# Kernel tuning notes

Measured on AMD Instinct MI355X. Metric: run time of the kernel, lower is better.

Reference implementation:

```python
import jax, jax.numpy as jnp
import numpy as np

N_NODES = 100000
N_EDGES = 800000


def gcn_conv(x, W, b, src, dst, ew, n):
    # PyG GCNConv with edge weights and self-loops already included in (src, dst, ew):
    # deg[i] = sum of incoming edge weights at i; norm_e = d^-1/2[src] * w_e * d^-1/2[dst]
    h = x @ W                                                  # [N, F_out]
    deg = jax.ops.segment_sum(ew, dst, num_segments=n)         # [N]
    dinv = jnp.where(deg > 0, jax.lax.rsqrt(deg), 0.0)
    norm = dinv[src] * ew * dinv[dst]                          # [E]
    out = jax.ops.segment_sum(h[src] * norm[:, None], dst, num_segments=n)
    return out + b


def add_self_loops(edge_index, edge_weight, n):
    loop = jnp.arange(n, dtype=edge_index.dtype)
    src = jnp.concatenate([edge_index[0], loop])
    dst = jnp.concatenate([edge_index[1], loop])
    ew = jnp.concatenate([edge_weight, jnp.ones((n,), edge_weight.dtype)])
    return src, dst, ew


def setup_inputs() -> dict:
    key = jax.random.key(0)
    ks = jax.random.split(key, 10)
    x = jax.random.normal(ks[0], (N_NODES, 5), jnp.float32)
    edge_index = jax.random.randint(ks[1], (2, N_EDGES), 0, N_NODES, dtype=jnp.int64)
    edge_weight = jax.random.uniform(ks[2], (N_EDGES,), jnp.float32)
    def glorot(k, fan_in, fan_out):
        s = float(np.sqrt(6.0 / (fan_in + fan_out)))
        return jax.random.uniform(k, (fan_in, fan_out), jnp.float32, -s, s)
    return {
        "x": x,
        "edge_index": edge_index,
        "edge_weight": edge_weight,
        "W1": glorot(ks[3], 5, 320),
        "b1": jnp.zeros((320,), jnp.float32),
        "W2": glorot(ks[4], 320, 160),
        "b2": jnp.zeros((160,), jnp.float32),
        "We": glorot(ks[5], 160, 80),
        "be": jnp.zeros((80,), jnp.float32),
    }


def reference(x, edge_index, edge_weight, W1, b1, W2, b2, We, be):
    n = x.shape[0]
    src, dst, ew = add_self_loops(edge_index, edge_weight, n)
    h = gcn_conv(x, W1, b1, src, dst, ew, n)        # conv1
    h = jax.nn.relu(h)
    h = gcn_conv(h, W2, b2, src, dst, ew, n)        # conv2
    return h @ We + be                              # embed linear
```

## Files before the change

### kernel.cpp

```cpp
#include <hip/hip_runtime.h>

#define NF0 5
#define F1 320
#define F2 160
#define F3 80
#define NSUB 8
#define SUBCAP 512

typedef float f32x4 __attribute__((ext_vector_type(4)));
typedef _Float16 f16x8 __attribute__((ext_vector_type(8)));


__global__ void k_init(int* __restrict__ zreg, int zwords,
                       const unsigned int* __restrict__ ei32, int E, int* __restrict__ flag) {
    for (int t = blockIdx.x * 256 + threadIdx.x; t < zwords; t += gridDim.x * 256)
        zreg[t] = 0;
    if (blockIdx.x == 0) {
        __shared__ int ok;
        if (threadIdx.x == 0) ok = 1;
        __syncthreads();
        int np = E < 2048 ? E : 2048;
        for (int i = threadIdx.x; i < np; i += 256)
            if (ei32[2 * i + 1] != 0u) ok = 0;
        __syncthreads();
        if (threadIdx.x == 0) *flag = ok;
    }
}


__global__ void k_binA(const void* ei, const float* __restrict__ ew, const int* __restrict__ flag,
                       int* __restrict__ bin_cnt , int2* __restrict__ bins,
                       int n_bins, int* __restrict__ ovf_n, int* __restrict__ ovf,
                       int ovf_cap, int E) {
    int e = blockIdx.x * blockDim.x + threadIdx.x;
    if (e >= E) return;
    int sub = blockIdx.x & (NSUB - 1);
    int s, d;
    if (*flag) {
        const long long* p = (const long long*)ei;
        s = (int)p[e]; d = (int)p[E + e];
    } else {
        const int* p = (const int*)ei;
        s = p[e]; d = p[E + e];
    }
    float w = ew[e];
    int b = d >> 8;
    int pos = atomicAdd(&bin_cnt[(sub * n_bins + b) * 4], 1);
    if (pos < SUBCAP) {
        int2 pk;
        pk.x = s | ((d & 255) << 24);
        pk.y = __float_as_int(w);
        bins[(size_t)b * (NSUB * SUBCAP) + sub * SUBCAP + pos] = pk;
    } else {
        int o = atomicAdd(ovf_n, 1);
        if (o < ovf_cap) {
            ovf[3 * o] = s; ovf[3 * o + 1] = d; ovf[3 * o + 2] = __float_as_int(w);
        }
    }
}


__global__ __launch_bounds__(512) void k_binB1x(const int2* __restrict__ bins,
                                                const int* __restrict__ bin_cnt, int n_bins,
                                                float* __restrict__ dinv,
                                                const int* __restrict__ ovf_n,
                                                const int* __restrict__ ovf, int ovf_cap, int N,
                                                const float* __restrict__ W2,
                                                const float* __restrict__ We,
                                                _Float16* __restrict__ Bh,
                                                const float* __restrict__ b2,
                                                const float* __restrict__ be,
                                                float* __restrict__ bc) {
    __shared__ float deg_l[256];
    int b = blockIdx.x, t = threadIdx.x;
    if (b >= n_bins) {
        int xb = b - n_bins;
        if (xb < 50) {
            int idx = xb * 512 + t;
            int fid = idx >> 9;
            int rem = idx & 511;
            int lane = rem >> 3, i = rem & 7;
            int kk = fid / 5, ct = fid - kk * 5;
            int col = ct * 16 + (lane & 15);
            int row = kk * 32 + (lane >> 4) * 8 + i;
            const float* wr = W2 + (size_t)row * F2;
            float acc = 0.f;
            #pragma unroll 4
            for (int m = 0; m < F2; m += 4) {
                float4 w4 = *(const float4*)(wr + m);
                acc += w4.x * We[m * F3 + col] + w4.y * We[(m + 1) * F3 + col]
                     + w4.z * We[(m + 2) * F3 + col] + w4.w * We[(m + 3) * F3 + col];
            }
            Bh[((size_t)fid * 64 + lane) * 8 + i] = (_Float16)acc;
        } else {
            if (t < F3) {
                float s = be[t];
                for (int k = 0; k < F2; ++k) s += b2[k] * We[k * F3 + t];
                bc[t] = s;
            }
        }
        return;
    }
    if (t < 256) deg_l[t] = 0.f;
    __syncthreads();
    int th = t >> 8;
    int tt = t & 255;
    for (int sp = 0; sp < NSUB; sp += 2) {
        int sub = sp + th;
        int ne = bin_cnt[(sub * n_bins + b) * 4]; if (ne > SUBCAP) ne = SUBCAP;
        const int2* bp = bins + (size_t)b * (NSUB * SUBCAP) + sub * SUBCAP;
        for (int j = tt; j < ne; j += 256) {
            int2 pk = bp[j];
            atomicAdd(&deg_l[((unsigned int)pk.x) >> 24], __int_as_float(pk.y));
        }
    }
    int n = *ovf_n; if (n > ovf_cap) n = ovf_cap;
    int lo = b * 256;
    for (int j = t; j < n; j += 512) {
        int d = ovf[3 * j + 1];
        if (d >= lo && d < lo + 256)
            atomicAdd(&deg_l[d - lo], __int_as_float(ovf[3 * j + 2]));
    }
    __syncthreads();
    int node = lo + t;
    if (t < 256 && node < N) dinv[node] = rsqrtf(1.0f + deg_l[t]);
}


__global__ __launch_bounds__(512) void k_binB2(const int2* __restrict__ bins,
                                               const int* __restrict__ bin_cnt, int n_bins,
                                               const float* __restrict__ dinv,
                                               const float* __restrict__ x,
                                               int* __restrict__ cnt, int2* __restrict__ bucket,
                                               int cap, float* __restrict__ agg1,
                                               int* __restrict__ ovf_n, int* __restrict__ ovf,
                                               int ovf_cap, int N) {
    __shared__ int cnt_l[256];
    __shared__ float acc_l[256 * NF0];
    int b = blockIdx.x, t = threadIdx.x;
    if (t < 256) cnt_l[t] = 0;
    for (int q = t; q < 256 * NF0; q += 512) acc_l[q] = 0.f;
    int nsnap = *ovf_n; if (nsnap > ovf_cap) nsnap = ovf_cap;
    __syncthreads();
    int lo = b * 256;

    for (int j = t; j < nsnap; j += 512) {
        int d = ovf[3 * j + 1];
        if (d >= lo && d < lo + 256) {
            int s = ovf[3 * j];
            float w = __int_as_float(ovf[3 * j + 2]) * dinv[s];
            const float* xs = x + (size_t)s * NF0;
            int dl = d - lo;
            #pragma unroll
            for (int f = 0; f < NF0; ++f)
                atomicAdd(&acc_l[dl * NF0 + f], xs[f] * w);
        }
    }

    int th = t >> 8;
    int tt = t & 255;
    for (int sp = 0; sp < NSUB; sp += 2) {
        int sub = sp + th;
        int ne = bin_cnt[(sub * n_bins + b) * 4]; if (ne > SUBCAP) ne = SUBCAP;
        const int2* bp = bins + (size_t)b * (NSUB * SUBCAP) + sub * SUBCAP;
        for (int j = tt; j < ne; j += 256) {
            int2 pk = bp[j];
            int s = pk.x & 0xFFFFFF;
            int dl = ((unsigned int)pk.x) >> 24;
            int node = lo + dl;
            int pos = atomicAdd(&cnt_l[dl], 1);
            if (pos < cap) {
                int2 out_pk; out_pk.x = s; out_pk.y = pk.y;
                bucket[(size_t)node * cap + pos] = out_pk;
            } else {
                int o = atomicAdd(ovf_n, 1);
                if (o < ovf_cap) { ovf[3 * o] = s; ovf[3 * o + 1] = node; ovf[3 * o + 2] = pk.y; }
            }
            float w = __int_as_float(pk.y) * dinv[s];
            const float* xs = x + (size_t)s * NF0;
            float4 sv = *(const float4*)xs;
            float s4 = xs[4];
            atomicAdd(&acc_l[dl * NF0 + 0], sv.x * w);
            atomicAdd(&acc_l[dl * NF0 + 1], sv.y * w);
            atomicAdd(&acc_l[dl * NF0 + 2], sv.z * w);
            atomicAdd(&acc_l[dl * NF0 + 3], sv.w * w);
            atomicAdd(&acc_l[dl * NF0 + 4], s4 * w);
        }
    }
    __syncthreads();

    int node = lo + t;
    if (t < 256 && node < N) {
        float di = dinv[node];
        float sc = di * di;
        const float* xn = x + (size_t)node * NF0;
        float* op = agg1 + (size_t)node * NF0;
        #pragma unroll
        for (int f = 0; f < NF0; ++f)
            op[f] = di * acc_l[t * NF0 + f] + sc * xn[f];
        int c = cnt_l[t]; if (c > cap) c = cap;
        cnt[node] = c;
    }
}


__global__ __launch_bounds__(512) void k_node(const float* __restrict__ agg1,
                                              const float* __restrict__ W1,
                                              const float* __restrict__ b1,
                                              const _Float16* __restrict__ Bh,
                                              const float* __restrict__ dinv,
                                              _Float16* __restrict__ g, int N) {
    __shared__ float W_l[6 * F1];
    __shared__ _Float16 B_l[50 * 64 * 8];
    int tid = threadIdx.x;
    if (tid < 480) {
        float4 v = (tid < 400) ? ((const float4*)W1)[tid] : ((const float4*)b1)[tid - 400];
        ((float4*)W_l)[tid] = v;
    }
    {
        const float4* src = (const float4*)Bh;
        float4* dst = (float4*)B_l;
        for (int i = tid; i < 3200; i += 512) dst[i] = src[i];
    }
    __syncthreads();

    int w = tid >> 6, l = tid & 63;
    int nl = l & 15, kg = l >> 4;
    int base = blockIdx.x * 128 + w * 16;
    int n0 = base + nl;

    float a0v[5] = {0.f, 0.f, 0.f, 0.f, 0.f};
    if (n0 < N) {
        const float* ap = agg1 + (size_t)n0 * NF0;
        #pragma unroll
        for (int j = 0; j < 5; ++j) a0v[j] = ap[j];
    }

    f32x4 zero = {0.f, 0.f, 0.f, 0.f};
    f32x4 acc[5] = {zero, zero, zero, zero, zero};
    const f16x8* blp = (const f16x8*)B_l;

    #pragma unroll
    for (int kk = 0; kk < 10; ++kk) {
        int k0 = kk * 32 + kg * 8;
        float v0[8];
        const float* bb = W_l + 5 * F1 + k0;
        #pragma unroll
        for (int i = 0; i < 8; ++i) v0[i] = bb[i];
        #pragma unroll
        for (int j = 0; j < 5; ++j) {
            const float* wp = W_l + j * F1 + k0;
            float aj0 = a0v[j];
            #pragma unroll
            for (int i = 0; i < 8; ++i) v0[i] += aj0 * wp[i];
        }
        f16x8 ah0;
        #pragma unroll
        for (int i = 0; i < 8; ++i)
            ah0[i] = (_Float16)fmaxf(v0[i], 0.f);
        #pragma unroll
        for (int ct = 0; ct < 5; ++ct) {
            f16x8 bf = blp[(kk * 5 + ct) * 64 + l];
            acc[ct] = __builtin_amdgcn_mfma_f32_16x16x32_f16(ah0, bf, acc[ct], 0, 0, 0);
        }
    }

    #pragma unroll
    for (int r = 0; r < 4; ++r) {
        int r0 = base + kg * 4 + r;
        if (r0 < N) {
            float dv = dinv[r0];
            #pragma unroll
            for (int ct = 0; ct < 5; ++ct)
                g[(size_t)r0 * F3 + ct * 16 + nl] = (_Float16)(acc[ct][r] * dv);
        }
    }
}


__global__ __launch_bounds__(256) void k_aggB(const _Float16* __restrict__ g,
                                              const float* __restrict__ dinv,
                                              const float* __restrict__ bc,
                                              const int* __restrict__ cnt,
                                              const int2* __restrict__ bucket, int cap,
                                              const int* __restrict__ ovf_n,
                                              const int* __restrict__ ovf, int ovf_cap,
                                              float* __restrict__ out, int N) {
    int t = blockIdx.x * blockDim.x + threadIdx.x;
    if (t >= 10 * N) return;
    int i = t / 10;
    int c = (t - i * 10) << 3;
    float acc[8];
    #pragma unroll
    for (int e = 0; e < 8; ++e) acc[e] = 0.f;
    int cn = cnt[i];
    const int4* row4 = (const int4*)(bucket + (size_t)i * cap);
    int j = 0;
    for (; j + 2 <= cn; j += 2) {
        int4 q = row4[j >> 1];
        float w0 = __int_as_float(q.y);
        float w1 = __int_as_float(q.w);
        f16x8 a0 = *(const f16x8*)(g + (size_t)q.x * F3 + c);
        f16x8 a1 = *(const f16x8*)(g + (size_t)q.z * F3 + c);
        #pragma unroll
        for (int e = 0; e < 8; ++e)
            acc[e] += (float)a0[e] * w0 + (float)a1[e] * w1;
    }
    if (j < cn) {
        int2 p0 = ((const int2*)row4)[j];
        float w0 = __int_as_float(p0.y);
        f16x8 a0 = *(const f16x8*)(g + (size_t)p0.x * F3 + c);
        #pragma unroll
        for (int e = 0; e < 8; ++e)
            acc[e] += (float)a0[e] * w0;
    }
    {
        int n = *ovf_n; if (n > ovf_cap) n = ovf_cap;
        for (int o = 0; o < n; ++o) {
            if (ovf[3 * o + 1] == i) {
                int s = ovf[3 * o];
                float w0 = __int_as_float(ovf[3 * o + 2]);
                f16x8 a0 = *(const f16x8*)(g + (size_t)s * F3 + c);
                #pragma unroll
                for (int e = 0; e < 8; ++e)
                    acc[e] += (float)a0[e] * w0;
            }
        }
    }
    float di = dinv[i];
    f16x8 u0 = *(const f16x8*)(g + (size_t)i * F3 + c);
    const f32x4* bp = (const f32x4*)(bc + c);
    f32x4 q0 = bp[0], q1 = bp[1];
    f32x4 o0, o1;
    o0.x = di * (acc[0] + (float)u0[0]) + q0.x;
    o0.y = di * (acc[1] + (float)u0[1]) + q0.y;
    o0.z = di * (acc[2] + (float)u0[2]) + q0.z;
    o0.w = di * (acc[3] + (float)u0[3]) + q0.w;
    o1.x = di * (acc[4] + (float)u0[4]) + q1.x;
    o1.y = di * (acc[5] + (float)u0[5]) + q1.y;
    o1.z = di * (acc[6] + (float)u0[6]) + q1.z;
    o1.w = di * (acc[7] + (float)u0[7]) + q1.w;
    f32x4* op = (f32x4*)(out + (size_t)i * F3 + c);
    __builtin_nontemporal_store(o0, op);
    __builtin_nontemporal_store(o1, op + 1);
}


static inline size_t align256(size_t x) { return (x + 255) & ~(size_t)255; }

extern "C" void kernel_launch(void* const* d_in, const int* in_sizes, int n_in,
                              void* d_out, int out_size, void* d_ws, size_t ws_size,
                              hipStream_t stream) {
    const float* x  = (const float*)d_in[0];
    const void*  ei = d_in[1];
    const float* ew = (const float*)d_in[2];
    const float* W1 = (const float*)d_in[3];
    const float* b1 = (const float*)d_in[4];
    const float* W2 = (const float*)d_in[5];
    const float* b2 = (const float*)d_in[6];
    const float* We = (const float*)d_in[7];
    const float* be = (const float*)d_in[8];
    float* out = (float*)d_out;

    int N = in_sizes[0] / NF0;
    int E = in_sizes[2];

    const int OVF_CAP = 131072;
    int n_bins = (N + 255) >> 8;

    char* p = (char*)d_ws;
    auto alloc = [&](size_t bytes) { char* r = p; p += align256(bytes); return r; };
    int*   flag  = (int*)alloc(4);
    int zwords = 16 + NSUB * n_bins * 4;
    int*   zreg  = (int*)alloc((size_t)zwords * 4);
    int*   ovf_n = zreg;
    int*   bin_cnt = zreg + 16;
    float* dinv  = (float*)alloc((size_t)N * 4);
    int*   cnt   = (int*)  alloc((size_t)N * 4);
    int*   ovf   = (int*)  alloc((size_t)OVF_CAP * 12);
    int2*  bins  = (int2*) alloc((size_t)n_bins * NSUB * SUBCAP * 8);
    float* agg1  = (float*)alloc((size_t)N * NF0 * 4);
    float* bc    = (float*)alloc((size_t)F3 * 4);
    _Float16* Bh = (_Float16*)alloc((size_t)50 * 64 * 8 * 2);
    _Float16* g  = (_Float16*)alloc((size_t)N * F3 * 2);

    size_t used = (size_t)(p - (char*)d_ws);
    int cap = 24;
    if (ws_size > used) {
        size_t avail = (ws_size - used) / ((size_t)N * 8);
        if (avail < (size_t)cap) cap = (int)avail;
    } else cap = 4;
    cap &= ~1;
    if (cap < 4) cap = 4;
    int2* bucket = (int2*)alloc((size_t)N * cap * 8);

    int eb   = (E + 255) / 256;
    int zb   = (zwords + 255) / 256;

    k_init<<<zb, 256, 0, stream>>>(zreg, zwords, (const unsigned int*)ei, E, flag);
    k_binA<<<eb, 256, 0, stream>>>(ei, ew, flag, bin_cnt, bins, n_bins, ovf_n, ovf, OVF_CAP, E);
    k_binB1x<<<n_bins + 51, 512, 0, stream>>>(bins, bin_cnt, n_bins, dinv, ovf_n, ovf, OVF_CAP, N,
                                              W2, We, Bh, b2, be, bc);
    k_binB2<<<n_bins, 512, 0, stream>>>(bins, bin_cnt, n_bins, dinv, x, cnt, bucket, cap,
                                        agg1, ovf_n, ovf, OVF_CAP, N);
    k_node<<<(N + 127) / 128, 512, 0, stream>>>(agg1, W1, b1, Bh, dinv, g, N);
    k_aggB<<<(10 * N + 255) / 256, 256, 0, stream>>>(g, dinv, bc, cnt, bucket, cap,
                                                     ovf_n, ovf, OVF_CAP, out, N);
}
```

Measured before the change: 155.2 us.

## Prescale node features by dinv into padded buffer; read W1 directly in k_node

k_binB1x now writes a per-node copy of x pre-multiplied by dinv, padded to 8 floats, so k_binB2's edge loop no longer gathers dinv[s] and reads aligned 32-byte rows. The self-loop term becomes di*(acc + xp). Separately, k_node drops its W1/b1 shared-memory staging, reads those weights through vector global loads (cache-resident), and adds an occupancy hint of 6. The cost is an extra 3.2MB buffer write and more global load traffic in k_node.

After: 171.3 us. +10.4%, slower.

```diff
diff --git a/kernel.cpp b/kernel.cpp
--- a/kernel.cpp
+++ b/kernel.cpp
@@ -63,6 +63,8 @@
 __global__ __launch_bounds__(512) void k_binB1x(const int2* __restrict__ bins,
                                                 const int* __restrict__ bin_cnt, int n_bins,
                                                 float* __restrict__ dinv,
+                                                const float* __restrict__ x,
+                                                float* __restrict__ xp,
                                                 const int* __restrict__ ovf_n,
                                                 const int* __restrict__ ovf, int ovf_cap, int N,
                                                 const float* __restrict__ W2,
@@ -123,14 +125,23 @@
     }
     __syncthreads();
     int node = lo + t;
-    if (t < 256 && node < N) dinv[node] = rsqrtf(1.0f + deg_l[t]);
+    if (t < 256 && node < N) {
+        float di = rsqrtf(1.0f + deg_l[t]);
+        dinv[node] = di;
+        const float* xn = x + (size_t)node * NF0;
+        float4 v;
+        v.x = xn[0] * di; v.y = xn[1] * di; v.z = xn[2] * di; v.w = xn[3] * di;
+        float* xr = xp + (size_t)node * 8;
+        *(float4*)xr = v;
+        xr[4] = xn[4] * di;
+    }
 }
 
 
 __global__ __launch_bounds__(512) void k_binB2(const int2* __restrict__ bins,
                                                const int* __restrict__ bin_cnt, int n_bins,
                                                const float* __restrict__ dinv,
-                                               const float* __restrict__ x,
+                                               const float* __restrict__ xp,
                                                int* __restrict__ cnt, int2* __restrict__ bucket,
                                                int cap, float* __restrict__ agg1,
                                                int* __restrict__ ovf_n, int* __restrict__ ovf,
@@ -148,8 +159,8 @@
         int d = ovf[3 * j + 1];
         if (d >= lo && d < lo + 256) {
             int s = ovf[3 * j];
-            float w = __int_as_float(ovf[3 * j + 2]) * dinv[s];
-            const float* xs = x + (size_t)s * NF0;
+            float w = __int_as_float(ovf[3 * j + 2]);
+            const float* xs = xp + (size_t)s * 8;
             int dl = d - lo;
             #pragma unroll
             for (int f = 0; f < NF0; ++f)
@@ -176,8 +187,8 @@
                 int o = atomicAdd(ovf_n, 1);
                 if (o < ovf_cap) { ovf[3 * o] = s; ovf[3 * o + 1] = node; ovf[3 * o + 2] = pk.y; }
             }
-            float w = __int_as_float(pk.y) * dinv[s];
-            const float* xs = x + (size_t)s * NF0;
+            float w = __int_as_float(pk.y);
+            const float* xs = xp + (size_t)s * 8;
             float4 sv = *(const float4*)xs;
             float s4 = xs[4];
             atomicAdd(&acc_l[dl * NF0 + 0], sv.x * w);
@@ -192,31 +203,25 @@
     int node = lo + t;
     if (t < 256 && node < N) {
         float di = dinv[node];
-        float sc = di * di;
-        const float* xn = x + (size_t)node * NF0;
+        const float* xn = xp + (size_t)node * 8;
         float* op = agg1 + (size_t)node * NF0;
         #pragma unroll
         for (int f = 0; f < NF0; ++f)
-            op[f] = di * acc_l[t * NF0 + f] + sc * xn[f];
+            op[f] = di * (acc_l[t * NF0 + f] + xn[f]);
         int c = cnt_l[t]; if (c > cap) c = cap;
         cnt[node] = c;
     }
 }
 
 
-__global__ __launch_bounds__(512) void k_node(const float* __restrict__ agg1,
-                                              const float* __restrict__ W1,
-                                              const float* __restrict__ b1,
-                                              const _Float16* __restrict__ Bh,
-                                              const float* __restrict__ dinv,
-                                              _Float16* __restrict__ g, int N) {
-    __shared__ float W_l[6 * F1];
+__global__ __launch_bounds__(512, 6) void k_node(const float* __restrict__ agg1,
+                                                 const float* __restrict__ W1,
+                                                 const float* __restrict__ b1,
+                                                 const _Float16* __restrict__ Bh,
+                                                 const float* __restrict__ dinv,
+                                                 _Float16* __restrict__ g, int N) {
     __shared__ _Float16 B_l[50 * 64 * 8];
     int tid = threadIdx.x;
-    if (tid < 480) {
-        float4 v = (tid < 400) ? ((const float4*)W1)[tid] : ((const float4*)b1)[tid - 400];
-        ((float4*)W_l)[tid] = v;
-    }
     {
         const float4* src = (const float4*)Bh;
         float4* dst = (float4*)B_l;
@@ -244,15 +249,19 @@
     for (int kk = 0; kk < 10; ++kk) {
         int k0 = kk * 32 + kg * 8;
         float v0[8];
-        const float* bb = W_l + 5 * F1 + k0;
-        #pragma unroll
-        for (int i = 0; i < 8; ++i) v0[i] = bb[i];
+        {
+            const float4* bp = (const float4*)(b1 + k0);
+            float4 q0 = bp[0], q1 = bp[1];
+            v0[0] = q0.x; v0[1] = q0.y; v0[2] = q0.z; v0[3] = q0.w;
+            v0[4] = q1.x; v0[5] = q1.y; v0[6] = q1.z; v0[7] = q1.w;
+        }
         #pragma unroll
         for (int j = 0; j < 5; ++j) {
-            const float* wp = W_l + j * F1 + k0;
+            const float4* wp = (const float4*)(W1 + j * F1 + k0);
+            float4 w0 = wp[0], w1 = wp[1];
             float aj0 = a0v[j];
-            #pragma unroll
-            for (int i = 0; i < 8; ++i) v0[i] += aj0 * wp[i];
+            v0[0] += aj0 * w0.x; v0[1] += aj0 * w0.y; v0[2] += aj0 * w0.z; v0[3] += aj0 * w0.w;
+            v0[4] += aj0 * w1.x; v0[5] += aj0 * w1.y; v0[6] += aj0 * w1.z; v0[7] += aj0 * w1.w;
         }
         f16x8 ah0;
         #pragma unroll
@@ -376,6 +385,7 @@
     int*   ovf_n = zreg;
     int*   bin_cnt = zreg + 16;
     float* dinv  = (float*)alloc((size_t)N * 4);
+    float* xp    = (float*)alloc((size_t)N * 8 * 4);
     int*   cnt   = (int*)  alloc((size_t)N * 4);
     int*   ovf   = (int*)  alloc((size_t)OVF_CAP * 12);
     int2*  bins  = (int2*) alloc((size_t)n_bins * NSUB * SUBCAP * 8);
@@ -399,9 +409,9 @@
 
     k_init<<<zb, 256, 0, stream>>>(zreg, zwords, (const unsigned int*)ei, E, flag);
     k_binA<<<eb, 256, 0, stream>>>(ei, ew, flag, bin_cnt, bins, n_bins, ovf_n, ovf, OVF_CAP, E);
-    k_binB1x<<<n_bins + 51, 512, 0, stream>>>(bins, bin_cnt, n_bins, dinv, ovf_n, ovf, OVF_CAP, N,
-                                              W2, We, Bh, b2, be, bc);
-    k_binB2<<<n_bins, 512, 0, stream>>>(bins, bin_cnt, n_bins, dinv, x, cnt, bucket, cap,
+    k_binB1x<<<n_bins + 51, 512, 0, stream>>>(bins, bin_cnt, n_bins, dinv, x, xp,
+                                              ovf_n, ovf, OVF_CAP, N, W2, We, Bh, b2, be, bc);
+    k_binB2<<<n_bins, 512, 0, stream>>>(bins, bin_cnt, n_bins, dinv, xp, cnt, bucket, cap,
                                         agg1, ovf_n, ovf, OVF_CAP, N);
     k_node<<<(N + 127) / 128, 512, 0, stream>>>(agg1, W1, b1, Bh, dinv, g, N);
     k_aggB<<<(10 * N + 255) / 256, 256, 0, stream>>>(g, dinv, bc, cnt, bucket, cap,
```
